# Performance work log

Hardware: AMD Instinct MI355X
Metric: run time of the kernel (lower is better)

The kernel has to match this reference:

```python
import jax, jax.numpy as jnp
import numpy as np

B, L, D, H = 2, 2048, 1024, 16
HD = D // H

def setup_inputs() -> dict:
    key = jax.random.key(0)
    ks = jax.random.split(key, 9)
    s = 1.0 / np.sqrt(D)
    return {
        "query": jax.random.normal(ks[0], (B, L, D), dtype=jnp.float32),
        "Wq": jax.random.uniform(ks[1], (D, D), jnp.float32, -s, s),
        "bq": jax.random.uniform(ks[2], (D,), jnp.float32, -s, s),
        "Wk": jax.random.uniform(ks[3], (D, D), jnp.float32, -s, s),
        "bk": jax.random.uniform(ks[4], (D,), jnp.float32, -s, s),
        "Wv": jax.random.uniform(ks[5], (D, D), jnp.float32, -s, s),
        "bv": jax.random.uniform(ks[6], (D,), jnp.float32, -s, s),
        "Wo": jax.random.uniform(ks[7], (D, D), jnp.float32, -s, s),
        "bo": jax.random.uniform(ks[8], (D,), jnp.float32, -s, s),
    }

def reference(query, Wq, bq, Wk, bk, Wv, bv, Wo, bo):
    # self-attention: key_value = query. Linear: x @ W.T + b (torch convention)
    scale = HD ** -0.5
    q = (query @ Wq.T + bq).reshape(B, L, H, HD).transpose(0, 2, 1, 3)  # (B,H,L,hd)
    k = (query @ Wk.T + bk).reshape(B, L, H, HD).transpose(0, 2, 1, 3)
    v = (query @ Wv.T + bv).reshape(B, L, H, HD).transpose(0, 2, 1, 3)
    logits = jnp.einsum('bhqd,bhkd->bhqk', q, k) * scale  # (B,H,Lq,Lk)
    attn = jax.nn.softmax(logits, axis=-1)
    out = jnp.einsum('bhqk,bhkd->bhqd', attn, v)
    out = out.transpose(0, 2, 1, 3).reshape(B, L, D)
    return out @ Wo.T + bo
```

## Files before the change

kernel.cpp:

```cpp
#include <hip/hip_runtime.h>

#define Bc 2
#define Lc 2048
#define Dc 1024
#define Hc 16
#define HDc 64
#define LOG2E 1.44269504088896340736f

typedef __bf16 bf16x8 __attribute__((ext_vector_type(8)));
typedef __bf16 bf16x2 __attribute__((ext_vector_type(2)));
typedef float f32x4 __attribute__((ext_vector_type(4)));
typedef unsigned short u16;
typedef unsigned int u32;
typedef unsigned long long u64;

__device__ __forceinline__ u16 f2bf(float x) {
    union { float f; u32 u; } c; c.f = x;
    u32 u = c.u + 0x7fffu + ((c.u >> 16) & 1u);
    return (u16)(u >> 16);
}

__device__ __forceinline__ u32 pkbf(float a, float b) {
#if __has_builtin(__builtin_amdgcn_cvt_pk_bf16_f32)
    union { bf16x2 v; u32 u; } c;
    c.v = __builtin_amdgcn_cvt_pk_bf16_f32(a, b);
    return c.u;
#else
    return (u32)f2bf(a) | ((u32)f2bf(b) << 16);
#endif
}

__device__ __forceinline__ void g2l16(const void* g, void* l) {
    __builtin_amdgcn_global_load_lds(
        (const __attribute__((address_space(1))) void*)g,
        (__attribute__((address_space(3))) void*)l, 16, 0, 0);
}

__global__ __launch_bounds__(256) void cast_bf16(
    const float* __restrict__ x,
    const float* __restrict__ wq, const float* __restrict__ wk,
    const float* __restrict__ wv, const float* __restrict__ wo,
    u16* __restrict__ xb, u16* __restrict__ wqb, u16* __restrict__ wkb,
    u16* __restrict__ wvb, u16* __restrict__ wob)
{
    const int i = blockIdx.x * 256 + threadIdx.x;
    const float* s; u16* d; int off;
    if (i < 1048576) { s = x; d = xb; off = i; }
    else {
        const int j = i - 1048576;
        const int sel = j >> 18;
        off = j & 262143;
        s = sel == 0 ? wq : sel == 1 ? wk : sel == 2 ? wv : wo;
        d = sel == 0 ? wqb : sel == 1 ? wkb : sel == 2 ? wvb : wob;
    }
    const float4 f = ((const float4*)s)[off];
    ushort4 o;
    o.x = f2bf(f.x); o.y = f2bf(f.y); o.z = f2bf(f.z); o.w = f2bf(f.w);
    ((ushort4*)d)[off] = o;
}

__device__ __forceinline__ void gemm128_body(
    const u16* __restrict__ A, const u16* __restrict__ Bm,
    int row0, int col0, int K,
    f32x4 (&acc)[4][4], u16* As, u16* Bs)
{
    const int tid  = threadIdx.x;
    const int w    = tid >> 6;
    const int lane = tid & 63;
    const int l15  = lane & 15, quad = lane >> 4;
    const int srow = lane >> 2;
    const int scol = (lane & 3) << 3;
    const int wm   = (w & 1) << 6, wn = (w >> 1) << 6;

    for (int k0 = 0; k0 < K; k0 += 32) {
        __syncthreads();
#pragma unroll
        for (int s = 0; s < 2; ++s) {
            const int r = w * 32 + s * 16;
            g2l16(&A [(size_t)(row0 + r + srow) * K + k0 + scol], &As[r * 32]);
            g2l16(&Bm[(size_t)(col0 + r + srow) * K + k0 + scol], &Bs[r * 32]);
        }
        __syncthreads();

        bf16x8 af[4], bf[4];
#pragma unroll
        for (int i = 0; i < 4; ++i)
            af[i] = *(const bf16x8*)&As[(wm + i * 16 + l15) * 32 + quad * 8];
#pragma unroll
        for (int j = 0; j < 4; ++j)
            bf[j] = *(const bf16x8*)&Bs[(wn + j * 16 + l15) * 32 + quad * 8];
#pragma unroll
        for (int i = 0; i < 4; ++i)
#pragma unroll
            for (int j = 0; j < 4; ++j)
                acc[i][j] = __builtin_amdgcn_mfma_f32_16x16x32_bf16(
                    af[i], bf[j], acc[i][j], 0, 0, 0);
    }
}

__global__ __launch_bounds__(256) void gemm_qkv_bf16(
    const u16* __restrict__ Xb,
    const u16* __restrict__ Wqb, const u16* __restrict__ Wkb, const u16* __restrict__ Wvb,
    const float* __restrict__ bq, const float* __restrict__ bk, const float* __restrict__ bv,
    u16* __restrict__ qo, u16* __restrict__ ko, u16* __restrict__ vto)
{
    __shared__ __attribute__((aligned(16))) u16 As[128 * 32];
    __shared__ __attribute__((aligned(16))) u16 Bs[128 * 32];

    const int z = blockIdx.z;
    const int tid = threadIdx.x;
    const int w = tid >> 6, lane = tid & 63;
    const int l15 = lane & 15, quad = lane >> 4;
    const int wm = (w & 1) << 6, wn = (w >> 1) << 6;

    f32x4 acc[4][4];
#pragma unroll
    for (int i = 0; i < 4; ++i)
#pragma unroll
        for (int j = 0; j < 4; ++j)
#pragma unroll
            for (int r = 0; r < 4; ++r) acc[i][j][r] = 0.0f;

    if (z == 2) {
        const int row0 = blockIdx.y << 7;
        const int col0 = blockIdx.x << 7;
        gemm128_body(Wvb, Xb, row0, col0, Dc, acc, As, Bs);

        float bvv[4][4];
#pragma unroll
        for (int i = 0; i < 4; ++i)
#pragma unroll
            for (int r = 0; r < 4; ++r)
                bvv[i][r] = bv[row0 + wm + i * 16 + quad * 4 + r];
#pragma unroll
        for (int j = 0; j < 4; ++j) {
            const int mcol = col0 + wn + j * 16 + l15;
            const int bb = mcol >> 11, ll = mcol & (Lc - 1);
#pragma unroll
            for (int i = 0; i < 4; ++i)
#pragma unroll
                for (int r = 0; r < 4; ++r) {
                    const int nrow = row0 + wm + i * 16 + quad * 4 + r;
                    const int hh = nrow >> 6, hd = nrow & 63;
                    vto[(((size_t)(bb * Hc + hh) * HDc + hd) << 11) + ll] =
                        f2bf(acc[i][j][r] + bvv[i][r]);
                }
        }
        return;
    }

    const u16*   W    = z == 0 ? Wqb : Wkb;
    const float* bias = z == 0 ? bq  : bk;
    const int row0 = blockIdx.x << 7;
    const int col0 = blockIdx.y << 7;
    gemm128_body(Xb, W, row0, col0, Dc, acc, As, Bs);

    const float qs = 0.125f * LOG2E;
#pragma unroll
    for (int j = 0; j < 4; ++j) {
        const int n  = col0 + wn + j * 16 + l15;
        const float bj = bias[n];
        const int hh = n >> 6, hd = n & 63;
#pragma unroll
        for (int i = 0; i < 4; ++i)
#pragma unroll
            for (int r = 0; r < 4; ++r) {
                const int m  = row0 + wm + i * 16 + quad * 4 + r;
                const int bb = m >> 11, ll = m & (Lc - 1);
                const float val = acc[i][j][r] + bj;
                const size_t idx = (((size_t)(bb * Hc + hh) * Lc + ll) << 6) + hd;
                if (z == 0) qo[idx] = f2bf(val * qs);
                else        ko[idx] = f2bf(val);
            }
    }
}

__global__ __launch_bounds__(256) void attn_mfma(
    const u16* __restrict__ q, const u16* __restrict__ k,
    const u16* __restrict__ vt, u16* __restrict__ out)
{
    __shared__ __attribute__((aligned(16))) u16 Ks[2][64 * 32];
    __shared__ __attribute__((aligned(16))) u16 Vs[2][64 * 32];

    const int tid = threadIdx.x;
    const int w = tid >> 6, lane = tid & 63;
    const int l15 = lane & 15, quad = lane >> 4;
    const int bh = blockIdx.x & 31;
    const int qt = blockIdx.x >> 5;
    const int h  = bh & (Hc - 1);
    const int b  = bh >> 4;
    const int l0 = qt << 6;

    const size_t bhs = (size_t)(b * Hc + h) * (Lc * HDc);
    const u16* qb = q  + bhs;
    const u16* kb = k  + bhs;
    const u16* vb = vt + bhs;

    bf16x8 qf0, qf1;
    {
        const size_t row = (size_t)(l0 + w * 16 + l15) * HDc;
        qf0 = *(const bf16x8*)&qb[row + quad * 8];
        qf1 = *(const bf16x8*)&qb[row + 32 + quad * 8];
    }

    const int srow  = lane >> 2;
    const int sunit = lane & 3;
    const int gd = (l15 >> 1) & 3;

    f32x4 oacc[4];
    float l_i = 0.0f;
#pragma unroll
    for (int dt = 0; dt < 4; ++dt)
#pragma unroll
        for (int r = 0; r < 4; ++r) oacc[dt][r] = 0.0f;

    for (int kt = 0; kt < Lc; kt += 64) {
        __syncthreads();
#pragma unroll
        for (int i = 0; i < 4; ++i) {
            const int c = w * 4 + i;
            const int p = (c >> 2) & 1, g = c & 3;
            const int row = g * 16 + srow;
            if (c < 8)
                g2l16(&kb[(size_t)(kt + row) * HDc + p * 32 +
                          ((sunit ^ ((row >> 1) & 3)) << 3)],
                      &Ks[p][g * 512]);
            else
                g2l16(&vb[(size_t)row * Lc + kt + p * 32 +
                          ((sunit ^ ((row >> 1) & 3)) << 3)],
                      &Vs[p][g * 512]);
        }
        __syncthreads();

        f32x4 st[4];
#pragma unroll
        for (int t = 0; t < 4; ++t) {
            const int j   = t * 16 + l15;
            const int off = j * 32 + ((quad ^ gd) << 3);
            const bf16x8 kf0 = *(const bf16x8*)&Ks[0][off];
            const bf16x8 kf1 = *(const bf16x8*)&Ks[1][off];
            f32x4 z = {0.0f, 0.0f, 0.0f, 0.0f};
            z = __builtin_amdgcn_mfma_f32_16x16x32_bf16(kf0, qf0, z, 0, 0, 0);
            st[t] = __builtin_amdgcn_mfma_f32_16x16x32_bf16(kf1, qf1, z, 0, 0, 0);
        }

        u32 pk[4][2];
        f32x4 s4 = {0.0f, 0.0f, 0.0f, 0.0f};
#pragma unroll
        for (int t = 0; t < 4; ++t) {
            f32x4 p;
#pragma unroll
            for (int r = 0; r < 4; ++r) p[r] = exp2f(st[t][r]);
            s4 += p;
            pk[t][0] = pkbf(p[0], p[1]);
            pk[t][1] = pkbf(p[2], p[3]);
        }
        l_i += s4[0] + s4[1] + s4[2] + s4[3];

#pragma unroll
        for (int cp = 0; cp < 2; ++cp) {
#pragma unroll
            for (int dt = 0; dt < 4; ++dt) {
                const int base = (dt * 16 + l15) * 32 + ((quad & 1) << 2);
                union { bf16x8 v; u64 d[2]; } vf;
                vf.d[0] = *(const u64*)&Vs[cp][base + (((quad >> 1) ^ gd) << 3)];
                vf.d[1] = *(const u64*)&Vs[cp][base + (((2 + (quad >> 1)) ^ gd) << 3)];
                union { bf16x8 v; u32 uw[4]; } pf;
                pf.uw[0] = pk[2 * cp][0];
                pf.uw[1] = pk[2 * cp][1];
                pf.uw[2] = pk[2 * cp + 1][0];
                pf.uw[3] = pk[2 * cp + 1][1];
                oacc[dt] = __builtin_amdgcn_mfma_f32_16x16x32_bf16(
                    vf.v, pf.v, oacc[dt], 0, 0, 0);
            }
        }
    }

    float l = l_i;
    l += __shfl_xor(l, 16);
    l += __shfl_xor(l, 32);
    const float inv = 1.0f / l;
    const int lrow = l0 + w * 16 + l15;
    u16* ob = out + ((size_t)(b * Lc + lrow)) * Dc + h * HDc;
#pragma unroll
    for (int dt = 0; dt < 4; ++dt) {
        uint2 pr;
        pr.x = pkbf(oacc[dt][0] * inv, oacc[dt][1] * inv);
        pr.y = pkbf(oacc[dt][2] * inv, oacc[dt][3] * inv);
        *(uint2*)&ob[dt * 16 + quad * 4] = pr;
    }
}

__global__ __launch_bounds__(256) void gemm_o_bf16(
    const u16* __restrict__ Ab, const u16* __restrict__ Wob,
    const float* __restrict__ bo, float* __restrict__ out)
{
    __shared__ __attribute__((aligned(16))) u16 As[128 * 32];
    __shared__ __attribute__((aligned(16))) u16 Bs[128 * 32];
    const int row0 = blockIdx.x << 7;
    const int col0 = blockIdx.y << 7;

    f32x4 acc[4][4];
#pragma unroll
    for (int i = 0; i < 4; ++i)
#pragma unroll
        for (int j = 0; j < 4; ++j)
#pragma unroll
            for (int r = 0; r < 4; ++r) acc[i][j][r] = 0.0f;

    gemm128_body(Ab, Wob, row0, col0, Dc, acc, As, Bs);

    const int tid = threadIdx.x;
    const int w = tid >> 6, lane = tid & 63;
    const int l15 = lane & 15, quad = lane >> 4;
    const int wm = (w & 1) << 6, wn = (w >> 1) << 6;

#pragma unroll
    for (int j = 0; j < 4; ++j) {
        const int n = col0 + wn + j * 16 + l15;
        const float bj = bo[n];
#pragma unroll
        for (int i = 0; i < 4; ++i)
#pragma unroll
            for (int r = 0; r < 4; ++r) {
                const int m = row0 + wm + i * 16 + quad * 4 + r;
                out[(size_t)m * Dc + n] = acc[i][j][r] + bj;
            }
    }
}

extern "C" void kernel_launch(void* const* d_in, const int* in_sizes, int n_in,
                              void* d_out, int out_size, void* d_ws, size_t ws_size,
                              hipStream_t stream)
{
    const float* query = (const float*)d_in[0];
    const float* Wq = (const float*)d_in[1];
    const float* bq = (const float*)d_in[2];
    const float* Wk = (const float*)d_in[3];
    const float* bk = (const float*)d_in[4];
    const float* Wv = (const float*)d_in[5];
    const float* bv = (const float*)d_in[6];
    const float* Wo = (const float*)d_in[7];
    const float* bo = (const float*)d_in[8];

    u16* ws = (u16*)d_ws;
    const size_t nX = (size_t)Bc * Lc * Dc;
    const size_t nW = (size_t)Dc * Dc;
    u16* xb  = ws;
    u16* wqb = xb + nX;
    u16* wkb = wqb + nW;
    u16* wvb = wkb + nW;
    u16* wob = wvb + nW;
    u16* q_w = wob + nW;
    u16* k_w = q_w + nX;
    u16* vt_w = k_w + nX;
    u16* a_w = vt_w + nX;

    cast_bf16<<<dim3(8192), 256, 0, stream>>>(query, Wq, Wk, Wv, Wo,
                                              xb, wqb, wkb, wvb, wob);
    gemm_qkv_bf16<<<dim3(32, 8, 3), 256, 0, stream>>>(xb, wqb, wkb, wvb,
                                                      bq, bk, bv, q_w, k_w, vt_w);
    attn_mfma<<<dim3(1024), 256, 0, stream>>>(q_w, k_w, vt_w, a_w);
    gemm_o_bf16<<<dim3(32, 8), 256, 0, stream>>>(a_w, wob, bo, (float*)d_out);
}
```

Measured before the change: 227.5 us.

## Process two 16-row query tiles per wave in attention kernel

Each wave now computes two 16-row query tiles instead of one, so a block covers 128 query rows and the grid is halved. Every K/V tile staged in shared memory and every V fragment read from LDS is reused for twice as many queries, cutting global and LDS load traffic per unit of work. In exchange, register use per thread rises and there are fewer blocks to spread across the compute units, which may reduce occupancy and latency hiding.

```diff
diff --git a/kernel.cpp b/kernel.cpp
--- a/kernel.cpp
+++ b/kernel.cpp
@@ -189,30 +189,33 @@
     const int qt = blockIdx.x >> 5;
     const int h  = bh & (Hc - 1);
     const int b  = bh >> 4;
-    const int l0 = qt << 6;
+    const int l0 = qt << 7;
 
     const size_t bhs = (size_t)(b * Hc + h) * (Lc * HDc);
     const u16* qb = q  + bhs;
     const u16* kb = k  + bhs;
     const u16* vb = vt + bhs;
 
-    bf16x8 qf0, qf1;
-    {
-        const size_t row = (size_t)(l0 + w * 16 + l15) * HDc;
-        qf0 = *(const bf16x8*)&qb[row + quad * 8];
-        qf1 = *(const bf16x8*)&qb[row + 32 + quad * 8];
+    bf16x8 qf[2][2];
+#pragma unroll
+    for (int mt = 0; mt < 2; ++mt) {
+        const size_t row = (size_t)(l0 + w * 32 + mt * 16 + l15) * HDc;
+        qf[mt][0] = *(const bf16x8*)&qb[row + quad * 8];
+        qf[mt][1] = *(const bf16x8*)&qb[row + 32 + quad * 8];
     }
 
     const int srow  = lane >> 2;
     const int sunit = lane & 3;
     const int gd = (l15 >> 1) & 3;
 
-    f32x4 oacc[4];
-    float l_i = 0.0f;
-#pragma unroll
-    for (int dt = 0; dt < 4; ++dt)
-#pragma unroll
-        for (int r = 0; r < 4; ++r) oacc[dt][r] = 0.0f;
+    f32x4 oacc[2][4];
+    float l_i[2] = {0.0f, 0.0f};
+#pragma unroll
+    for (int mt = 0; mt < 2; ++mt)
+#pragma unroll
+        for (int dt = 0; dt < 4; ++dt)
+#pragma unroll
+            for (int r = 0; r < 4; ++r) oacc[mt][dt][r] = 0.0f;
 
     for (int kt = 0; kt < Lc; kt += 64) {
         __syncthreads();
@@ -232,62 +235,73 @@
         }
         __syncthreads();
 
-        f32x4 st[4];
+        f32x4 st[2][4];
 #pragma unroll
         for (int t = 0; t < 4; ++t) {
             const int j   = t * 16 + l15;
             const int off = j * 32 + ((quad ^ gd) << 3);
             const bf16x8 kf0 = *(const bf16x8*)&Ks[0][off];
             const bf16x8 kf1 = *(const bf16x8*)&Ks[1][off];
-            f32x4 z = {0.0f, 0.0f, 0.0f, 0.0f};
-            z = __builtin_amdgcn_mfma_f32_16x16x32_bf16(kf0, qf0, z, 0, 0, 0);
-            st[t] = __builtin_amdgcn_mfma_f32_16x16x32_bf16(kf1, qf1, z, 0, 0, 0);
-        }
-
-        u32 pk[4][2];
-        f32x4 s4 = {0.0f, 0.0f, 0.0f, 0.0f};
-#pragma unroll
-        for (int t = 0; t < 4; ++t) {
-            f32x4 p;
-#pragma unroll
-            for (int r = 0; r < 4; ++r) p[r] = exp2f(st[t][r]);
-            s4 += p;
-            pk[t][0] = pkbf(p[0], p[1]);
-            pk[t][1] = pkbf(p[2], p[3]);
-        }
-        l_i += s4[0] + s4[1] + s4[2] + s4[3];
+#pragma unroll
+            for (int mt = 0; mt < 2; ++mt) {
+                f32x4 z = {0.0f, 0.0f, 0.0f, 0.0f};
+                z = __builtin_amdgcn_mfma_f32_16x16x32_bf16(kf0, qf[mt][0], z, 0, 0, 0);
+                st[mt][t] = __builtin_amdgcn_mfma_f32_16x16x32_bf16(kf1, qf[mt][1], z, 0, 0, 0);
+            }
+        }
+
+        u32 pk[2][4][2];
+#pragma unroll
+        for (int mt = 0; mt < 2; ++mt) {
+            f32x4 s4 = {0.0f, 0.0f, 0.0f, 0.0f};
+#pragma unroll
+            for (int t = 0; t < 4; ++t) {
+                f32x4 p;
+#pragma unroll
+                for (int r = 0; r < 4; ++r) p[r] = exp2f(st[mt][t][r]);
+                s4 += p;
+                pk[mt][t][0] = pkbf(p[0], p[1]);
+                pk[mt][t][1] = pkbf(p[2], p[3]);
+            }
+            l_i[mt] += s4[0] + s4[1] + s4[2] + s4[3];
+        }
 
 #pragma unroll
         for (int cp = 0; cp < 2; ++cp) {
+            union { bf16x8 v; u32 uw[4]; } pf0, pf1;
+            pf0.uw[0] = pk[0][2 * cp][0];     pf0.uw[1] = pk[0][2 * cp][1];
+            pf0.uw[2] = pk[0][2 * cp + 1][0]; pf0.uw[3] = pk[0][2 * cp + 1][1];
+            pf1.uw[0] = pk[1][2 * cp][0];     pf1.uw[1] = pk[1][2 * cp][1];
+            pf1.uw[2] = pk[1][2 * cp + 1][0]; pf1.uw[3] = pk[1][2 * cp + 1][1];
 #pragma unroll
             for (int dt = 0; dt < 4; ++dt) {
                 const int base = (dt * 16 + l15) * 32 + ((quad & 1) << 2);
                 union { bf16x8 v; u64 d[2]; } vf;
                 vf.d[0] = *(const u64*)&Vs[cp][base + (((quad >> 1) ^ gd) << 3)];
                 vf.d[1] = *(const u64*)&Vs[cp][base + (((2 + (quad >> 1)) ^ gd) << 3)];
-                union { bf16x8 v; u32 uw[4]; } pf;
-                pf.uw[0] = pk[2 * cp][0];
-                pf.uw[1] = pk[2 * cp][1];
-                pf.uw[2] = pk[2 * cp + 1][0];
-                pf.uw[3] = pk[2 * cp + 1][1];
-                oacc[dt] = __builtin_amdgcn_mfma_f32_16x16x32_bf16(
-                    vf.v, pf.v, oacc[dt], 0, 0, 0);
-            }
-        }
-    }
-
-    float l = l_i;
-    l += __shfl_xor(l, 16);
-    l += __shfl_xor(l, 32);
-    const float inv = 1.0f / l;
-    const int lrow = l0 + w * 16 + l15;
-    u16* ob = out + ((size_t)(b * Lc + lrow)) * Dc + h * HDc;
-#pragma unroll
-    for (int dt = 0; dt < 4; ++dt) {
-        uint2 pr;
-        pr.x = pkbf(oacc[dt][0] * inv, oacc[dt][1] * inv);
-        pr.y = pkbf(oacc[dt][2] * inv, oacc[dt][3] * inv);
-        *(uint2*)&ob[dt * 16 + quad * 4] = pr;
+                oacc[0][dt] = __builtin_amdgcn_mfma_f32_16x16x32_bf16(
+                    vf.v, pf0.v, oacc[0][dt], 0, 0, 0);
+                oacc[1][dt] = __builtin_amdgcn_mfma_f32_16x16x32_bf16(
+                    vf.v, pf1.v, oacc[1][dt], 0, 0, 0);
+            }
+        }
+    }
+
+#pragma unroll
+    for (int mt = 0; mt < 2; ++mt) {
+        float l = l_i[mt];
+        l += __shfl_xor(l, 16);
+        l += __shfl_xor(l, 32);
+        const float inv = 1.0f / l;
+        const int lrow = l0 + w * 32 + mt * 16 + l15;
+        u16* ob = out + ((size_t)(b * Lc + lrow)) * Dc + h * HDc;
+#pragma unroll
+        for (int dt = 0; dt < 4; ++dt) {
+            uint2 pr;
+            pr.x = pkbf(oacc[mt][dt][0] * inv, oacc[mt][dt][1] * inv);
+            pr.y = pkbf(oacc[mt][dt][2] * inv, oacc[mt][dt][3] * inv);
+            *(uint2*)&ob[dt * 16 + quad * 4] = pr;
+        }
     }
 }
 
@@ -360,6 +374,6 @@
                                               xb, wqb, wkb, wvb, wob);
     gemm_qkv_bf16<<<dim3(32, 8, 3), 256, 0, stream>>>(xb, wqb, wkb, wvb,
                                                       bq, bk, bv, q_w, k_w, vt_w);
-    attn_mfma<<<dim3(1024), 256, 0, stream>>>(q_w, k_w, vt_w, a_w);
+    attn_mfma<<<dim3(512), 256, 0, stream>>>(q_w, k_w, vt_w, a_w);
     gemm_o_bf16<<<dim3(32, 8), 256, 0, stream>>>(a_w, wob, bo, (float*)d_out);
 }
```

Result: no change. 228.2 us (+0.3%).
